# Performance work log

Measured on AMD Instinct MI355X. Metric: run time of the kernel, lower is better.

## Reference

```python
import jax, jax.numpy as jnp
import numpy as np

B, N, DIM = 4, 2048, 64  # batch, seq_len (== gate out dim), model dim (== dim_head)
H, DH = 8, 64            # heads, dim_head


def setup_inputs() -> dict:
    key = jax.random.key(0)
    ks = jax.random.split(key, 12)
    inner = H * DH
    inp = {
        'q': jax.random.normal(ks[0], (B, N, DIM), jnp.float32),
        'k': jax.random.normal(ks[1], (B, N, DIM), jnp.float32),
        'v': jax.random.normal(ks[2], (B, N, DIM), jnp.float32),
        'Wq': jax.random.normal(ks[3], (inner, DIM), jnp.float32) * 0.05,
        'Wk': jax.random.normal(ks[4], (inner, DIM), jnp.float32) * 0.05,
        'Wv': jax.random.normal(ks[5], (inner, DIM), jnp.float32) * 0.05,
        'Wo': jax.random.normal(ks[6], (DIM, inner), jnp.float32) * 0.05,
        'bo': jax.random.normal(ks[7], (DIM,), jnp.float32) * 0.05,
        'Wg': jax.random.normal(ks[8], (N, DIM), jnp.float32) * 0.05,
        's_local': jnp.float32(1.0),
        's_long': jnp.float32(1.0),
        # recurrent compressive-memory state; positive to avoid 0/0 of zero-init buffers
        'mem': jax.random.uniform(ks[9], (H, DH, DH), jnp.float32) + 0.5,
        'mem_norm': jax.random.uniform(ks[10], (H, N, 1), jnp.float32) + 0.5,
    }
    return inp


def _heads(x, W):
    # x: (B,N,DIM) @ W.T (DIM, H*DH) -> (B,H,N,DH)
    y = x @ W.T
    return y.reshape(x.shape[0], x.shape[1], H, DH).transpose(0, 2, 1, 3)


def reference(q, k, v, Wq, Wk, Wv, Wo, bo, Wg, s_local, s_long, mem, mem_norm):
    scale = DH ** -0.5
    qh, kh, vh = _heads(q, Wq), _heads(k, Wk), _heads(v, Wv)  # (B,H,N,DH)

    # local softmax attention, down-gated by (1 - sigmoid(local scalar))
    sim = jnp.einsum('bhnd,bhmd->bhnm', qh, kh) * scale
    local_attn = jax.nn.softmax(sim, axis=-1) * (1.0 - jax.nn.sigmoid(s_local))

    # query compressive memory: elu(q) @ M / (elu(q) * norm)
    eq = jax.nn.elu(qh)
    mem_q = jnp.einsum('bhnd,hde->bhne', eq, mem) / (eq * mem_norm[None])  # (B,H,N,DH)
    gated = jax.nn.sigmoid(s_long) * jnp.einsum('bhnd,md->bhnm', mem_q, Wg)  # (B,H,N,N)

    attn = local_attn + gated
    out = jnp.einsum('bhnm,bhmd->bhnd', attn, vh)
    out = out.transpose(0, 2, 1, 3).reshape(q.shape[0], q.shape[1], H * DH)
    out = out @ Wo.T + bo  # (B,N,DIM)

    # memory update (state side effect in the original forward)
    ek = jax.nn.elu(kh)
    v_term = vh - jnp.einsum('bhnd,hde->bhne', ek, mem) / (ek * mem_norm[None])
    new_mem = mem[None] + jnp.einsum('bhnd,bhne->bhde', ek, v_term)  # (B,H,DH,DH)
    new_norm = ek.sum(-1)  # (B,H,N)
    return out, new_mem, new_norm
```

## Files before the change

### kernel.cpp

```cpp
#include <hip/hip_runtime.h>
#include <math.h>


#define B_   4
#define N_   2048
#define H_   8
#define BH_  32
#define KP   72
#define SCLK 0.18033688f

typedef __bf16 bf16x8 __attribute__((ext_vector_type(8)));
typedef __bf16 bf16x4 __attribute__((ext_vector_type(4)));
typedef short  s16x4  __attribute__((ext_vector_type(4)));
typedef float  f32x4  __attribute__((ext_vector_type(4)));

__device__ __forceinline__ float eluf(float x) {
    return x > 0.0f ? x : expm1f(x);
}

__device__ __forceinline__ float fexp2(float x) {
    return __builtin_amdgcn_exp2f(x);
}

__device__ __forceinline__ f32x4 mfma16(bf16x4 a, bf16x4 b, f32x4 c) {
#if __has_builtin(__builtin_amdgcn_mfma_f32_16x16x16_bf16)
    return __builtin_amdgcn_mfma_f32_16x16x16_bf16(a, b, c, 0, 0, 0);
#else
    s16x4 ai, bi;
    __builtin_memcpy(&ai, &a, 8);
    __builtin_memcpy(&bi, &b, 8);
    return __builtin_amdgcn_mfma_f32_16x16x16bf16_1k(ai, bi, c, 0, 0, 0);
#endif
}

__global__ __launch_bounds__(256) void k_proj(
    const float* __restrict__ q, const float* __restrict__ k, const float* __restrict__ v,
    const float* __restrict__ Wq, const float* __restrict__ Wk, const float* __restrict__ Wv,
    __bf16* __restrict__ qb, float* __restrict__ kh, __bf16* __restrict__ kb,
    __bf16* __restrict__ vb, __bf16* __restrict__ vbT)
{
    const int which = blockIdx.z;
    const int h    = blockIdx.y;
    const int row0 = blockIdx.x * 64;
    const int tid  = threadIdx.x;
    const int b = row0 >> 11, nb = row0 & 2047;

    __shared__ __align__(16) float  AsT[64][68];
    __shared__ __align__(16) float  WsT[64][68];
    __shared__ __align__(16) __bf16 Cs[64 * 72];

    if (which == 2) {
        const int w = tid >> 6, lane = tid & 63;
        const int quad = lane >> 4, m = lane & 15;
        const float* ar = v + (size_t)(row0 + w * 16 + m) * 64;
        bf16x8 a0, a1;
        #pragma unroll
        for (int j = 0; j < 8; ++j) {
            a0[j] = (__bf16)ar[quad * 8 + j];
            a1[j] = (__bf16)ar[32 + quad * 8 + j];
        }
        f32x4 acc[4];
        #pragma unroll
        for (int t = 0; t < 4; ++t) {
            const float* wr = Wv + (size_t)(h * 64 + t * 16 + m) * 64;
            bf16x8 b0, b1;
            #pragma unroll
            for (int j = 0; j < 8; ++j) {
                b0[j] = (__bf16)wr[quad * 8 + j];
                b1[j] = (__bf16)wr[32 + quad * 8 + j];
            }
            f32x4 z = {0.f, 0.f, 0.f, 0.f};
            z = __builtin_amdgcn_mfma_f32_16x16x32_bf16(a0, b0, z, 0, 0, 0);
            acc[t] = __builtin_amdgcn_mfma_f32_16x16x32_bf16(a1, b1, z, 0, 0, 0);
        }
        #pragma unroll
        for (int t = 0; t < 4; ++t)
            #pragma unroll
            for (int r = 0; r < 4; ++r)
                Cs[(w * 16 + quad * 4 + r) * 72 + t * 16 + m] = (__bf16)acc[t][r];
        __syncthreads();
        const int rr = tid >> 2, csg = (tid & 3) * 16;
        bf16x8 r0 = *(const bf16x8*)&Cs[rr * 72 + csg];
        bf16x8 r1 = *(const bf16x8*)&Cs[rr * 72 + csg + 8];
        size_t gb = ((((size_t)b * H_ + h) * N_ + nb + rr) << 6) + csg;
        *(bf16x8*)&vb[gb]     = r0;
        *(bf16x8*)&vb[gb + 8] = r1;
        const int e = tid >> 2, ns = (tid & 3) * 16;
        bf16x8 t0, t1;
        #pragma unroll
        for (int j = 0; j < 8; ++j) {
            t0[j] = Cs[(ns + j) * 72 + e];
            t1[j] = Cs[(ns + 8 + j) * 72 + e];
        }
        size_t base = (((size_t)b * H_ + h) * 64 + e) * (size_t)N_ + nb + ns;
        *(bf16x8*)&vbT[base]     = t0;
        *(bf16x8*)&vbT[base + 8] = t1;
        return;
    }

    const float* __restrict__ src = (which == 0) ? q : k;
    const float* __restrict__ W   = (which == 0) ? Wq : Wk;
    for (int s = 0; s < 16; ++s) {
        int flat = s * 256 + tid;
        int r = flat >> 6, d = flat & 63;
        AsT[d][r] = src[(size_t)(row0 + r) * 64 + d];
        WsT[d][r] = W[(size_t)(h * 64 + r) * 64 + d];
    }
    __syncthreads();

    const int ty = tid >> 4, tx = tid & 15;
    float acc[4][4];
    #pragma unroll
    for (int i = 0; i < 4; ++i)
        #pragma unroll
        for (int j = 0; j < 4; ++j) acc[i][j] = 0.0f;
    for (int kd = 0; kd < 64; ++kd) {
        float4 a4 = *(const float4*)&AsT[kd][ty * 4];
        float4 w4 = *(const float4*)&WsT[kd][tx * 4];
        float a[4] = {a4.x, a4.y, a4.z, a4.w};
        float w[4] = {w4.x, w4.y, w4.z, w4.w};
        #pragma unroll
        for (int i = 0; i < 4; ++i)
            #pragma unroll
            for (int j = 0; j < 4; ++j) acc[i][j] = fmaf(a[i], w[j], acc[i][j]);
    }

    if (which == 0) {
        #pragma unroll
        for (int i = 0; i < 4; ++i) {
            size_t idx = ((((size_t)b * H_ + h) * N_ + nb + ty * 4 + i) << 6) + tx * 4;
            bf16x4 o4 = {(__bf16)acc[i][0], (__bf16)acc[i][1],
                         (__bf16)acc[i][2], (__bf16)acc[i][3]};
            *(bf16x4*)&qb[idx] = o4;
        }
    } else {
        #pragma unroll
        for (int i = 0; i < 4; ++i) {
            size_t idx = ((((size_t)b * H_ + h) * N_ + nb + ty * 4 + i) << 6) + tx * 4;
            *(float4*)&kh[idx] = make_float4(acc[i][0], acc[i][1], acc[i][2], acc[i][3]);
            bf16x4 o4 = {(__bf16)(acc[i][0] * SCLK), (__bf16)(acc[i][1] * SCLK),
                         (__bf16)(acc[i][2] * SCLK), (__bf16)(acc[i][3] * SCLK)};
            *(bf16x4*)&kb[idx] = o4;
        }
    }
}

__global__ __launch_bounds__(256) void k_memacc(
    const float* __restrict__ kh, const __bf16* __restrict__ vb,
    const float* __restrict__ mem, const float* __restrict__ mem_norm,
    float* __restrict__ pmem, float* __restrict__ out_norm)
{
    const int chunk = blockIdx.x;
    const int bh    = blockIdx.y;
    const int h     = bh & 7;
    const int n0    = chunk * 128;

    __shared__ __align__(16) __bf16 memT_hi[64 * KP], memT_lo[64 * KP];
    __shared__ __align__(16) __bf16 ekn_hi[64 * KP],  ekn_lo[64 * KP];
    __shared__ __align__(16) __bf16 ekT_hi[64 * KP],  ekT_lo[64 * KP];
    __shared__ __align__(16) __bf16 vtT_hi[64 * KP],  vtT_lo[64 * KP];

    const int tid  = threadIdx.x;
    const int w    = tid >> 6, lane = tid & 63;
    const int quad = lane >> 4, m = lane & 15;

    for (int s = 0; s < 16; ++s) {
        int flat = s * 256 + tid;
        int d = flat >> 6, e = flat & 63;
        float mv = mem[(size_t)h * 4096 + flat];
        __bf16 hi = (__bf16)mv;
        memT_hi[e * KP + d] = hi;
        memT_lo[e * KP + d] = (__bf16)(mv - (float)hi);
    }

    bf16x8 onesv;
    #pragma unroll
    for (int j = 0; j < 8; ++j) onesv[j] = (m == 0) ? (__bf16)1.0f : (__bf16)0.0f;

    f32x4 accM[4];
    #pragma unroll
    for (int t = 0; t < 4; ++t) { f32x4 z = {0.f, 0.f, 0.f, 0.f}; accM[t] = z; }
    __syncthreads();

    for (int sub = 0; sub < 2; ++sub) {
        const int nb = n0 + sub * 64;
        for (int rr = w; rr < 64; rr += 4) {
            const int n = nb + rr;
            float ekv = eluf(kh[((size_t)bh * N_ + n) * 64 + lane]);
            __bf16 hi = (__bf16)ekv;
            __bf16 lo = (__bf16)(ekv - (float)hi);
            ekn_hi[rr * KP + lane] = hi;
            ekn_lo[rr * KP + lane] = lo;
            ekT_hi[lane * KP + rr] = hi;
            ekT_lo[lane * KP + rr] = lo;
        }
        __syncthreads();

        f32x4 km[4];
        #pragma unroll
        for (int t = 0; t < 4; ++t) { f32x4 z = {0.f, 0.f, 0.f, 0.f}; km[t] = z; }
        f32x4 nsum = {0.f, 0.f, 0.f, 0.f};
        #pragma unroll
        for (int c2 = 0; c2 < 2; ++c2) {
            bf16x8 Ah = *(const bf16x8*)&ekn_hi[(w * 16 + m) * KP + c2 * 32 + quad * 8];
            bf16x8 Al = *(const bf16x8*)&ekn_lo[(w * 16 + m) * KP + c2 * 32 + quad * 8];
            nsum = __builtin_amdgcn_mfma_f32_16x16x32_bf16(Ah, onesv, nsum, 0, 0, 0);
            nsum = __builtin_amdgcn_mfma_f32_16x16x32_bf16(Al, onesv, nsum, 0, 0, 0);
            #pragma unroll
            for (int et = 0; et < 4; ++et) {
                bf16x8 Bh = *(const bf16x8*)&memT_hi[(et * 16 + m) * KP + c2 * 32 + quad * 8];
                bf16x8 Bl = *(const bf16x8*)&memT_lo[(et * 16 + m) * KP + c2 * 32 + quad * 8];
                km[et] = __builtin_amdgcn_mfma_f32_16x16x32_bf16(Al, Bh, km[et], 0, 0, 0);
                km[et] = __builtin_amdgcn_mfma_f32_16x16x32_bf16(Ah, Bl, km[et], 0, 0, 0);
                km[et] = __builtin_amdgcn_mfma_f32_16x16x32_bf16(Ah, Bh, km[et], 0, 0, 0);
            }
        }
        if (m == 0) {
            #pragma unroll
            for (int r = 0; r < 4; ++r)
                out_norm[(size_t)bh * N_ + nb + w * 16 + quad * 4 + r] = nsum[r];
        }
        float nrmv[4];
        #pragma unroll
        for (int r = 0; r < 4; ++r)
            nrmv[r] = mem_norm[(size_t)h * N_ + nb + w * 16 + quad * 4 + r];
        #pragma unroll
        for (int et = 0; et < 4; ++et) {
            #pragma unroll
            for (int r = 0; r < 4; ++r) {
                const int nl = w * 16 + quad * 4 + r;
                const int e  = et * 16 + m;
                float vh  = (float)vb[((size_t)bh * N_ + nb + nl) * 64 + e];
                float ekv = (float)ekn_hi[nl * KP + e] + (float)ekn_lo[nl * KP + e];
                float vt  = vh - km[et][r] * __builtin_amdgcn_rcpf(ekv * nrmv[r]);
                __bf16 hi = (__bf16)vt;
                vtT_hi[e * KP + nl] = hi;
                vtT_lo[e * KP + nl] = (__bf16)(vt - (float)hi);
            }
        }
        __syncthreads();

        #pragma unroll
        for (int c2 = 0; c2 < 2; ++c2) {
            bf16x8 Ah = *(const bf16x8*)&ekT_hi[(w * 16 + m) * KP + c2 * 32 + quad * 8];
            bf16x8 Al = *(const bf16x8*)&ekT_lo[(w * 16 + m) * KP + c2 * 32 + quad * 8];
            #pragma unroll
            for (int et = 0; et < 4; ++et) {
                bf16x8 Bh = *(const bf16x8*)&vtT_hi[(et * 16 + m) * KP + c2 * 32 + quad * 8];
                bf16x8 Bl = *(const bf16x8*)&vtT_lo[(et * 16 + m) * KP + c2 * 32 + quad * 8];
                accM[et] = __builtin_amdgcn_mfma_f32_16x16x32_bf16(Al, Bh, accM[et], 0, 0, 0);
                accM[et] = __builtin_amdgcn_mfma_f32_16x16x32_bf16(Ah, Bl, accM[et], 0, 0, 0);
                accM[et] = __builtin_amdgcn_mfma_f32_16x16x32_bf16(Ah, Bh, accM[et], 0, 0, 0);
            }
        }
        __syncthreads();
    }

    const size_t base = ((size_t)chunk * BH_ + bh) * 4096;
    #pragma unroll
    for (int et = 0; et < 4; ++et)
        #pragma unroll
        for (int r = 0; r < 4; ++r)
            pmem[base + (size_t)(w * 16 + quad * 4 + r) * 64 + et * 16 + m] =
                accM[et][r];
}

__global__ __launch_bounds__(256) void k_gv(
    const float* __restrict__ Wg, const __bf16* __restrict__ vbT,
    float* __restrict__ pGv)
{
    const int chunk = blockIdx.x;
    const int bh    = blockIdx.y;
    const int n0    = chunk * 128;
    __shared__ __align__(16) __bf16 WgT[64 * 136];
    const int tid  = threadIdx.x;
    const int w    = tid >> 6, lane = tid & 63;
    const int quad = lane >> 4, m = tid & 15;

    for (int s = 0; s < 8; ++s) {
        int f4 = s * 256 + tid;
        int n = f4 >> 4, dg = (f4 & 15) * 4;
        float4 wv = *(const float4*)&Wg[(size_t)(n0 + n) * 64 + dg];
        WgT[(dg + 0) * 136 + n] = (__bf16)wv.x;
        WgT[(dg + 1) * 136 + n] = (__bf16)wv.y;
        WgT[(dg + 2) * 136 + n] = (__bf16)wv.z;
        WgT[(dg + 3) * 136 + n] = (__bf16)wv.w;
    }
    __syncthreads();

    f32x4 acc[4];
    #pragma unroll
    for (int t = 0; t < 4; ++t) { f32x4 z = {0.f, 0.f, 0.f, 0.f}; acc[t] = z; }
    #pragma unroll
    for (int c = 0; c < 4; ++c) {
        bf16x8 Af = *(const bf16x8*)&WgT[(w * 16 + m) * 136 + c * 32 + quad * 8];
        #pragma unroll
        for (int et = 0; et < 4; ++et) {
            bf16x8 Bf = *(const bf16x8*)&vbT[((size_t)bh * 64 + et * 16 + m) * N_ +
                                             n0 + c * 32 + quad * 8];
            acc[et] = __builtin_amdgcn_mfma_f32_16x16x32_bf16(Af, Bf, acc[et], 0, 0, 0);
        }
    }
    const size_t base = ((size_t)chunk * BH_ + bh) * 4096;
    #pragma unroll
    for (int et = 0; et < 4; ++et)
        #pragma unroll
        for (int r = 0; r < 4; ++r)
            pGv[base + (size_t)(w * 16 + quad * 4 + r) * 64 + et * 16 + m] =
                acc[et][r];
}

__global__ __launch_bounds__(256) void k_reduce(
    const float* __restrict__ mem, const float* __restrict__ pmem,
    const float* __restrict__ pGv, float* __restrict__ out_mem, float* __restrict__ Gv)
{
    const int idx = blockIdx.x * 256 + threadIdx.x;
    const int bh = idx >> 12, h = bh & 7, de = idx & 4095;
    float sm = mem[(size_t)h * 4096 + de];
    float sg = 0.0f;
    #pragma unroll
    for (int c = 0; c < 16; ++c) {
        sm += pmem[(size_t)c * 131072 + idx];
        sg += pGv[(size_t)c * 131072 + idx];
    }
    out_mem[idx] = sm;
    Gv[idx] = sg;
}

__global__ __launch_bounds__(256, 4) void k_flash(
    const __bf16* __restrict__ qb, const __bf16* __restrict__ kb,
    const __bf16* __restrict__ vbT, const float* __restrict__ mem,
    const float* __restrict__ mem_norm, const float* __restrict__ Gv,
    const float* __restrict__ s_local_p, const float* __restrict__ s_long_p,
    __bf16* __restrict__ o)
{
    const int n0 = blockIdx.x * 128;
    const int bh = blockIdx.y;
    const int h  = bh & 7;
    const __bf16* __restrict__ kbp = kb  + (size_t)bh * N_ * 64;
    const __bf16* __restrict__ vtp = vbT + (size_t)bh * 64 * N_;

    __shared__ __align__(16) __bf16 Kb[64 * KP];
    __shared__ __align__(16) __bf16 VT[64 * KP];
    __shared__ __align__(16) __bf16 Pw[128 * KP];
    __shared__ float lsl[128];
    __shared__ float nrm_l[128];

    const int tid  = threadIdx.x;
    const int w    = tid >> 6, lane = tid & 63;
    const int quad = lane >> 4, m = lane & 15;
    const float gl   = 1.0f - 1.0f / (1.0f + __expf(-s_local_p[0]));
    const float sigg = 1.0f / (1.0f + __expf(-s_long_p[0]));

    if (tid < 128) nrm_l[tid] = mem_norm[(size_t)h * N_ + n0 + tid];

    const size_t q0 = ((size_t)bh * N_ + n0 + w * 32 + m) * 64;
    const size_t q1 = q0 + 16 * 64;
    bf16x8 qa00 = *(const bf16x8*)&qb[q0 + quad * 8];
    bf16x8 qa01 = *(const bf16x8*)&qb[q0 + 32 + quad * 8];
    bf16x8 qa10 = *(const bf16x8*)&qb[q1 + quad * 8];
    bf16x8 qa11 = *(const bf16x8*)&qb[q1 + 32 + quad * 8];

    f32x4 O0[4], O1[4];
    #pragma unroll
    for (int t = 0; t < 4; ++t) {
        f32x4 z = {0.f, 0.f, 0.f, 0.f};
        O0[t] = z; O1[t] = z;
    }
    float lsum0 = 0.f, lsum1 = 0.f;
    const int pr0 = w * 32, pr1 = w * 32 + 16;

    const int srow = tid >> 2, scg = (tid & 3) * 16;
    bf16x8 pk0 = *(const bf16x8*)&kbp[(size_t)srow * 64 + scg];
    bf16x8 pk1 = *(const bf16x8*)&kbp[(size_t)srow * 64 + scg + 8];
    bf16x8 pv0 = *(const bf16x8*)&vtp[(size_t)srow * N_ + scg];
    bf16x8 pv1 = *(const bf16x8*)&vtp[(size_t)srow * N_ + scg + 8];

    for (int c = 0; c < 32; ++c) {
        __syncthreads();
        *(bf16x8*)&Kb[srow * KP + scg]     = pk0;
        *(bf16x8*)&Kb[srow * KP + scg + 8] = pk1;
        *(bf16x8*)&VT[srow * KP + scg]     = pv0;
        *(bf16x8*)&VT[srow * KP + scg + 8] = pv1;
        __syncthreads();
        if (c + 1 < 32) {
            const size_t kn = (size_t)((c + 1) * 64 + srow) * 64 + scg;
            const size_t vn = (size_t)srow * N_ + (c + 1) * 64 + scg;
            pk0 = *(const bf16x8*)&kbp[kn];
            pk1 = *(const bf16x8*)&kbp[kn + 8];
            pv0 = *(const bf16x8*)&vtp[vn];
            pv1 = *(const bf16x8*)&vtp[vn + 8];
        }

        f32x4 s0[4], s1[4];
        #pragma unroll
        for (int t = 0; t < 4; ++t) {
            bf16x8 ka0 = *(const bf16x8*)&Kb[(t * 16 + m) * KP + quad * 8];
            bf16x8 ka1 = *(const bf16x8*)&Kb[(t * 16 + m) * KP + 32 + quad * 8];
            f32x4 z = {0.f, 0.f, 0.f, 0.f};
            z = __builtin_amdgcn_mfma_f32_16x16x32_bf16(ka0, qa00, z, 0, 0, 0);
            s0[t] = __builtin_amdgcn_mfma_f32_16x16x32_bf16(ka1, qa01, z, 0, 0, 0);
            f32x4 z2 = {0.f, 0.f, 0.f, 0.f};
            z2 = __builtin_amdgcn_mfma_f32_16x16x32_bf16(ka0, qa10, z2, 0, 0, 0);
            s1[t] = __builtin_amdgcn_mfma_f32_16x16x32_bf16(ka1, qa11, z2, 0, 0, 0);
        }

        bf16x4 pa0[4], pa1[4];
        #pragma unroll
        for (int t = 0; t < 4; ++t) {
            float p0 = fexp2(s0[t][0]), p1 = fexp2(s0[t][1]);
            float p2 = fexp2(s0[t][2]), p3 = fexp2(s0[t][3]);
            lsum0 += p0 + p1 + p2 + p3;
            bf16x4 pk = {(__bf16)p0, (__bf16)p1, (__bf16)p2, (__bf16)p3};
            pa0[t] = pk;
            float r0 = fexp2(s1[t][0]), r1 = fexp2(s1[t][1]);
            float r2 = fexp2(s1[t][2]), r3 = fexp2(s1[t][3]);
            lsum1 += r0 + r1 + r2 + r3;
            bf16x4 rk = {(__bf16)r0, (__bf16)r1, (__bf16)r2, (__bf16)r3};
            pa1[t] = rk;
        }

        #pragma unroll
        for (int t = 0; t < 4; ++t) {
            #pragma unroll
            for (int et = 0; et < 4; ++et) {
                bf16x4 vb4 = *(const bf16x4*)&VT[(et * 16 + m) * KP + t * 16 + quad * 4];
                O0[et] = mfma16(pa0[t], vb4, O0[et]);
                O1[et] = mfma16(pa1[t], vb4, O1[et]);
            }
        }
    }

    lsum0 += __shfl_xor(lsum0, 16, 64); lsum0 += __shfl_xor(lsum0, 32, 64);
    lsum1 += __shfl_xor(lsum1, 16, 64); lsum1 += __shfl_xor(lsum1, 32, 64);
    if (lane < 16) { lsl[pr0 + lane] = lsum0; lsl[pr1 + lane] = lsum1; }

    __syncthreads();
    for (int s2 = 0; s2 < 16; ++s2) {
        int flat = s2 * 256 + tid;
        int d = flat >> 6, e = flat & 63;
        Kb[e * KP + d] = (__bf16)mem[(size_t)h * 4096 + flat];
        VT[e * KP + d] = (__bf16)Gv[(size_t)bh * 4096 + flat];
    }
    __syncthreads();

    __bf16* op = o + ((size_t)bh * N_ + n0) * 64;
    #pragma unroll
    for (int s = 0; s < 2; ++s) {
        const int prs = w * 32 + s * 16;
        bf16x8 ea0, ea1;
        #pragma unroll
        for (int j = 0; j < 8; ++j) {
            ea0[j] = (__bf16)eluf((float)(s == 0 ? qa00[j] : qa10[j]));
            ea1[j] = (__bf16)eluf((float)(s == 0 ? qa01[j] : qa11[j]));
        }
        f32x4 num[4];
        #pragma unroll
        for (int t = 0; t < 4; ++t) {
            bf16x8 b0 = *(const bf16x8*)&Kb[(t * 16 + m) * KP + quad * 8];
            bf16x8 b1 = *(const bf16x8*)&Kb[(t * 16 + m) * KP + 32 + quad * 8];
            f32x4 z = {0.f, 0.f, 0.f, 0.f};
            z = __builtin_amdgcn_mfma_f32_16x16x32_bf16(ea0, b0, z, 0, 0, 0);
            num[t] = __builtin_amdgcn_mfma_f32_16x16x32_bf16(ea1, b1, z, 0, 0, 0);
        }
        *(bf16x8*)&Pw[(prs + m) * KP + quad * 8]      = ea0;
        *(bf16x8*)&Pw[(prs + m) * KP + 32 + quad * 8] = ea1;
        asm volatile("s_waitcnt lgkmcnt(0)" ::: "memory");
        float mq[4][4];
        #pragma unroll
        for (int t = 0; t < 4; ++t)
            #pragma unroll
            for (int r = 0; r < 4; ++r) {
                float eqv = (float)Pw[(prs + quad * 4 + r) * KP + t * 16 + m];
                mq[t][r] = num[t][r] / (eqv * nrm_l[prs + quad * 4 + r]);
            }
        #pragma unroll
        for (int t = 0; t < 4; ++t)
            #pragma unroll
            for (int r = 0; r < 4; ++r)
                Pw[(prs + quad * 4 + r) * KP + t * 16 + m] = (__bf16)mq[t][r];
        asm volatile("s_waitcnt lgkmcnt(0)" ::: "memory");
        bf16x8 ma0 = *(const bf16x8*)&Pw[(prs + m) * KP + quad * 8];
        bf16x8 ma1 = *(const bf16x8*)&Pw[(prs + m) * KP + 32 + quad * 8];

        #pragma unroll
        for (int t = 0; t < 4; ++t) {
            bf16x8 g0 = *(const bf16x8*)&VT[(t * 16 + m) * KP + quad * 8];
            bf16x8 g1 = *(const bf16x8*)&VT[(t * 16 + m) * KP + 32 + quad * 8];
            f32x4 z = {0.f, 0.f, 0.f, 0.f};
            z = __builtin_amdgcn_mfma_f32_16x16x32_bf16(ma0, g0, z, 0, 0, 0);
            f32x4 o2 = __builtin_amdgcn_mfma_f32_16x16x32_bf16(ma1, g1, z, 0, 0, 0);
            #pragma unroll
            for (int r = 0; r < 4; ++r) {
                const int qr = prs + quad * 4 + r;
                float val = ((s == 0) ? O0[t][r] : O1[t][r]) * (gl / lsl[qr])
                            + sigg * o2[r];
                op[(size_t)qr * 64 + t * 16 + m] = (__bf16)val;
            }
        }
    }
}

__global__ __launch_bounds__(256) void k_outproj(
    const __bf16* __restrict__ o, const float* __restrict__ Wo,
    const float* __restrict__ bo, float* __restrict__ out)
{
    const int row0 = blockIdx.x * 64;
    const int b = row0 >> 11, nb = row0 & 2047;
    __shared__ __align__(16) __bf16 WoS[64 * 40];
    const int tid  = threadIdx.x;
    const int w    = tid >> 6, lane = tid & 63;
    const int quad = lane >> 4, m = lane & 15;

    f32x4 acc[4];
    #pragma unroll
    for (int t = 0; t < 4; ++t) { f32x4 z = {0.f, 0.f, 0.f, 0.f}; acc[t] = z; }

    for (int kbk = 0; kbk < 16; ++kbk) {
        for (int s2 = 0; s2 < 8; ++s2) {
            int flat = s2 * 256 + tid;
            int n = flat >> 5, kk = flat & 31;
            WoS[n * 40 + kk] = (__bf16)Wo[(size_t)n * 512 + kbk * 32 + kk];
        }
        __syncthreads();
        const int hc = kbk >> 1;
        size_t arow = (((size_t)b * H_ + hc) * N_ + nb + w * 16 + m);
        bf16x8 af = *(const bf16x8*)&o[arow * 64 + (kbk & 1) * 32 + quad * 8];
        #pragma unroll
        for (int t = 0; t < 4; ++t) {
            bf16x8 bf_ = *(const bf16x8*)&WoS[(t * 16 + m) * 40 + quad * 8];
            acc[t] = __builtin_amdgcn_mfma_f32_16x16x32_bf16(af, bf_, acc[t], 0, 0, 0);
        }
        __syncthreads();
    }
    #pragma unroll
    for (int t = 0; t < 4; ++t) {
        float bias = bo[t * 16 + m];
        #pragma unroll
        for (int r = 0; r < 4; ++r)
            out[(size_t)(row0 + w * 16 + quad * 4 + r) * 64 + t * 16 + m] =
                acc[t][r] + bias;
    }
}

extern "C" void kernel_launch(void* const* d_in, const int* in_sizes, int n_in,
                              void* d_out, int out_size, void* d_ws, size_t ws_size,
                              hipStream_t stream)
{
    const float* q        = (const float*)d_in[0];
    const float* k        = (const float*)d_in[1];
    const float* v        = (const float*)d_in[2];
    const float* Wq       = (const float*)d_in[3];
    const float* Wk       = (const float*)d_in[4];
    const float* Wv       = (const float*)d_in[5];
    const float* Wo       = (const float*)d_in[6];
    const float* bo       = (const float*)d_in[7];
    const float* Wg       = (const float*)d_in[8];
    const float* s_local  = (const float*)d_in[9];
    const float* s_long   = (const float*)d_in[10];
    const float* mem      = (const float*)d_in[11];
    const float* mem_norm = (const float*)d_in[12];

    float* ws = (float*)d_ws;
    float*  kh  = ws;
    __bf16* qb  = (__bf16*)(ws + 4194304);
    __bf16* kb  = (__bf16*)(ws + 6291456);
    __bf16* vb  = (__bf16*)(ws + 8388608);
    __bf16* vbT = (__bf16*)(ws + 10485760);
    float*  Gv  = ws + 12582912;
    float*  pm  = ws + 12713984;
    float*  pg  = ws + 14811136;
    __bf16* o   = (__bf16*)(ws + 12713984);

    float* out      = (float*)d_out;
    float* out_mem  = out + 524288;
    float* out_norm = out + 655360;

    k_proj   <<<dim3(128, 8, 3), 256, 0, stream>>>(q, k, v, Wq, Wk, Wv,
                                                   qb, kh, kb, vb, vbT);
    k_memacc <<<dim3(16, 32),    256, 0, stream>>>(kh, vb, mem, mem_norm,
                                                   pm, out_norm);
    k_gv     <<<dim3(16, 32),    256, 0, stream>>>(Wg, vbT, pg);
    k_reduce <<<dim3(512),       256, 0, stream>>>(mem, pm, pg, out_mem, Gv);
    k_flash  <<<dim3(16, 32),    256, 0, stream>>>(qb, kb, vbT, mem, mem_norm, Gv,
                                                   s_local, s_long, o);
    k_outproj<<<dim3(128),       256, 0, stream>>>(o, Wo, bo, out);
}
```

Before: 207.7 us.

## Use 512 threads per flash block with one 16-row tile per wave

The flash kernel now launches 512 threads (8 waves) per 128-query block, and each wave handles 16 query rows instead of 32. This halves per-thread accumulators and MFMA work and spreads tile staging across more threads. The idea is to raise wave-level parallelism and latency hiding. The V tile gets a different LDS padding, and the mem/Gv transpose load is rewritten to do vectorized bf16x4 LDS stores. In exchange, K/V tile loads are shared by more waves, each wave does less work per barrier, and register pressure under launch_bounds(512,4) may constrain the compiler.

```diff
diff --git a/kernel.cpp b/kernel.cpp
--- a/kernel.cpp
+++ b/kernel.cpp
@@ -7,6 +7,7 @@
 #define H_   8
 #define BH_  32
 #define KP   72
+#define KPV  68
 #define SCLK 0.18033688f
 
 typedef __bf16 bf16x8 __attribute__((ext_vector_type(8)));
@@ -327,7 +328,7 @@
     Gv[idx] = sg;
 }
 
-__global__ __launch_bounds__(256, 4) void k_flash(
+__global__ __launch_bounds__(512, 4) void k_flash(
     const __bf16* __restrict__ qb, const __bf16* __restrict__ kb,
     const __bf16* __restrict__ vbT, const float* __restrict__ mem,
     const float* __restrict__ mem_norm, const float* __restrict__ Gv,
@@ -341,7 +342,7 @@
     const __bf16* __restrict__ vtp = vbT + (size_t)bh * 64 * N_;
 
     __shared__ __align__(16) __bf16 Kb[64 * KP];
-    __shared__ __align__(16) __bf16 VT[64 * KP];
+    __shared__ __align__(16) __bf16 VT[64 * KPV];
     __shared__ __align__(16) __bf16 Pw[128 * KP];
     __shared__ float lsl[128];
     __shared__ float nrm_l[128];
@@ -354,45 +355,33 @@
 
     if (tid < 128) nrm_l[tid] = mem_norm[(size_t)h * N_ + n0 + tid];
 
-    const size_t q0 = ((size_t)bh * N_ + n0 + w * 32 + m) * 64;
-    const size_t q1 = q0 + 16 * 64;
+    const size_t q0 = ((size_t)bh * N_ + n0 + w * 16 + m) * 64;
     bf16x8 qa00 = *(const bf16x8*)&qb[q0 + quad * 8];
     bf16x8 qa01 = *(const bf16x8*)&qb[q0 + 32 + quad * 8];
-    bf16x8 qa10 = *(const bf16x8*)&qb[q1 + quad * 8];
-    bf16x8 qa11 = *(const bf16x8*)&qb[q1 + 32 + quad * 8];
-
-    f32x4 O0[4], O1[4];
-    #pragma unroll
-    for (int t = 0; t < 4; ++t) {
-        f32x4 z = {0.f, 0.f, 0.f, 0.f};
-        O0[t] = z; O1[t] = z;
-    }
-    float lsum0 = 0.f, lsum1 = 0.f;
-    const int pr0 = w * 32, pr1 = w * 32 + 16;
-
-    const int srow = tid >> 2, scg = (tid & 3) * 16;
+
+    f32x4 O0[4];
+    #pragma unroll
+    for (int t = 0; t < 4; ++t) { f32x4 z = {0.f, 0.f, 0.f, 0.f}; O0[t] = z; }
+    float lsum0 = 0.f;
+    const int prs = w * 16;
+
+    const int srow = tid >> 3, scg = (tid & 7) * 8;
     bf16x8 pk0 = *(const bf16x8*)&kbp[(size_t)srow * 64 + scg];
-    bf16x8 pk1 = *(const bf16x8*)&kbp[(size_t)srow * 64 + scg + 8];
     bf16x8 pv0 = *(const bf16x8*)&vtp[(size_t)srow * N_ + scg];
-    bf16x8 pv1 = *(const bf16x8*)&vtp[(size_t)srow * N_ + scg + 8];
 
     for (int c = 0; c < 32; ++c) {
         __syncthreads();
-        *(bf16x8*)&Kb[srow * KP + scg]     = pk0;
-        *(bf16x8*)&Kb[srow * KP + scg + 8] = pk1;
-        *(bf16x8*)&VT[srow * KP + scg]     = pv0;
-        *(bf16x8*)&VT[srow * KP + scg + 8] = pv1;
+        *(bf16x8*)&Kb[srow * KP + scg]  = pk0;
+        *(bf16x8*)&VT[srow * KPV + scg] = pv0;
         __syncthreads();
         if (c + 1 < 32) {
             const size_t kn = (size_t)((c + 1) * 64 + srow) * 64 + scg;
             const size_t vn = (size_t)srow * N_ + (c + 1) * 64 + scg;
             pk0 = *(const bf16x8*)&kbp[kn];
-            pk1 = *(const bf16x8*)&kbp[kn + 8];
             pv0 = *(const bf16x8*)&vtp[vn];
-            pv1 = *(const bf16x8*)&vtp[vn + 8];
-        }
-
-        f32x4 s0[4], s1[4];
+        }
+
+        f32x4 s0[4];
         #pragma unroll
         for (int t = 0; t < 4; ++t) {
             bf16x8 ka0 = *(const bf16x8*)&Kb[(t * 16 + m) * KP + quad * 8];
@@ -400,12 +389,9 @@
             f32x4 z = {0.f, 0.f, 0.f, 0.f};
             z = __builtin_amdgcn_mfma_f32_16x16x32_bf16(ka0, qa00, z, 0, 0, 0);
             s0[t] = __builtin_amdgcn_mfma_f32_16x16x32_bf16(ka1, qa01, z, 0, 0, 0);
-            f32x4 z2 = {0.f, 0.f, 0.f, 0.f};
-            z2 = __builtin_amdgcn_mfma_f32_16x16x32_bf16(ka0, qa10, z2, 0, 0, 0);
-            s1[t] = __builtin_amdgcn_mfma_f32_16x16x32_bf16(ka1, qa11, z2, 0, 0, 0);
-        }
-
-        bf16x4 pa0[4], pa1[4];
+        }
+
+        bf16x4 pa0[4];
         #pragma unroll
         for (int t = 0; t < 4; ++t) {
             float p0 = fexp2(s0[t][0]), p1 = fexp2(s0[t][1]);
@@ -413,46 +399,49 @@
             lsum0 += p0 + p1 + p2 + p3;
             bf16x4 pk = {(__bf16)p0, (__bf16)p1, (__bf16)p2, (__bf16)p3};
             pa0[t] = pk;
-            float r0 = fexp2(s1[t][0]), r1 = fexp2(s1[t][1]);
-            float r2 = fexp2(s1[t][2]), r3 = fexp2(s1[t][3]);
-            lsum1 += r0 + r1 + r2 + r3;
-            bf16x4 rk = {(__bf16)r0, (__bf16)r1, (__bf16)r2, (__bf16)r3};
-            pa1[t] = rk;
         }
 
         #pragma unroll
         for (int t = 0; t < 4; ++t) {
             #pragma unroll
             for (int et = 0; et < 4; ++et) {
-                bf16x4 vb4 = *(const bf16x4*)&VT[(et * 16 + m) * KP + t * 16 + quad * 4];
+                bf16x4 vb4 = *(const bf16x4*)&VT[(et * 16 + m) * KPV + t * 16 + quad * 4];
                 O0[et] = mfma16(pa0[t], vb4, O0[et]);
-                O1[et] = mfma16(pa1[t], vb4, O1[et]);
-            }
-        }
-    }
-
-    lsum0 += __shfl_xor(lsum0, 16, 64); lsum0 += __shfl_xor(lsum0, 32, 64);
-    lsum1 += __shfl_xor(lsum1, 16, 64); lsum1 += __shfl_xor(lsum1, 32, 64);
-    if (lane < 16) { lsl[pr0 + lane] = lsum0; lsl[pr1 + lane] = lsum1; }
+            }
+        }
+    }
+
+    lsum0 += __shfl_xor(lsum0, 16, 64);
+    lsum0 += __shfl_xor(lsum0, 32, 64);
+    if (lane < 16) lsl[prs + lane] = lsum0;
 
     __syncthreads();
-    for (int s2 = 0; s2 < 16; ++s2) {
-        int flat = s2 * 256 + tid;
-        int d = flat >> 6, e = flat & 63;
-        Kb[e * KP + d] = (__bf16)mem[(size_t)h * 4096 + flat];
-        VT[e * KP + d] = (__bf16)Gv[(size_t)bh * 4096 + flat];
+    {
+        const float* mp = mem + (size_t)h * 4096;
+        const float* gp = Gv + (size_t)bh * 4096;
+        #pragma unroll
+        for (int s2 = 0; s2 < 2; ++s2) {
+            int idx = s2 * 512 + tid;
+            int e = idx & 63, d4 = (idx >> 6) << 2;
+            bf16x4 mv, gv;
+            #pragma unroll
+            for (int j = 0; j < 4; ++j) {
+                mv[j] = (__bf16)mp[(size_t)(d4 + j) * 64 + e];
+                gv[j] = (__bf16)gp[(size_t)(d4 + j) * 64 + e];
+            }
+            *(bf16x4*)&Kb[e * KP + d4]  = mv;
+            *(bf16x4*)&VT[e * KPV + d4] = gv;
+        }
     }
     __syncthreads();
 
     __bf16* op = o + ((size_t)bh * N_ + n0) * 64;
-    #pragma unroll
-    for (int s = 0; s < 2; ++s) {
-        const int prs = w * 32 + s * 16;
+    {
         bf16x8 ea0, ea1;
         #pragma unroll
         for (int j = 0; j < 8; ++j) {
-            ea0[j] = (__bf16)eluf((float)(s == 0 ? qa00[j] : qa10[j]));
-            ea1[j] = (__bf16)eluf((float)(s == 0 ? qa01[j] : qa11[j]));
+            ea0[j] = (__bf16)eluf((float)qa00[j]);
+            ea1[j] = (__bf16)eluf((float)qa01[j]);
         }
         f32x4 num[4];
         #pragma unroll
@@ -485,16 +474,15 @@
 
         #pragma unroll
         for (int t = 0; t < 4; ++t) {
-            bf16x8 g0 = *(const bf16x8*)&VT[(t * 16 + m) * KP + quad * 8];
-            bf16x8 g1 = *(const bf16x8*)&VT[(t * 16 + m) * KP + 32 + quad * 8];
+            bf16x8 g0 = *(const bf16x8*)&VT[(t * 16 + m) * KPV + quad * 8];
+            bf16x8 g1 = *(const bf16x8*)&VT[(t * 16 + m) * KPV + 32 + quad * 8];
             f32x4 z = {0.f, 0.f, 0.f, 0.f};
             z = __builtin_amdgcn_mfma_f32_16x16x32_bf16(ma0, g0, z, 0, 0, 0);
             f32x4 o2 = __builtin_amdgcn_mfma_f32_16x16x32_bf16(ma1, g1, z, 0, 0, 0);
             #pragma unroll
             for (int r = 0; r < 4; ++r) {
                 const int qr = prs + quad * 4 + r;
-                float val = ((s == 0) ? O0[t][r] : O1[t][r]) * (gl / lsl[qr])
-                            + sigg * o2[r];
+                float val = O0[t][r] * (gl / lsl[qr]) + sigg * o2[r];
                 op[(size_t)qr * 64 + t * 16 + m] = (__bf16)val;
             }
         }
@@ -582,7 +570,7 @@
                                                    pm, out_norm);
     k_gv     <<<dim3(16, 32),    256, 0, stream>>>(Wg, vbT, pg);
     k_reduce <<<dim3(512),       256, 0, stream>>>(mem, pm, pg, out_mem, Gv);
-    k_flash  <<<dim3(16, 32),    256, 0, stream>>>(qb, kb, vbT, mem, mem_norm, Gv,
+    k_flash  <<<dim3(16, 32),    512, 0, stream>>>(qb, kb, vbT, mem, mem_norm, Gv,
                                                    s_local, s_long, o);
     k_outproj<<<dim3(128),       256, 0, stream>>>(o, Wo, bo, out);
 }
```

After: 201.2 us. -3.2%, faster.

## Double-buffer K/V tiles in flash kernel and enlarge blocks to 512 threads

Applied to the files above, without the earlier changes.

The flash-attention kernel now processes 256 query rows per 512-thread block. K and V^T tiles sit in ping-pong LDS buffers, so each key chunk needs one barrier instead of two, and global prefetch runs two chunks ahead. The V tile uses a narrower padding stride, and the memory/Gv transpose into LDS is rewritten to issue 4-element vector stores. LDS is carved from one shared byte array with aliased regions for the epilogue. The larger LDS footprint and bigger blocks reduce block count and may limit occupancy.

```diff
diff --git a/kernel.cpp b/kernel.cpp
--- a/kernel.cpp
+++ b/kernel.cpp
@@ -7,6 +7,7 @@
 #define H_   8
 #define BH_  32
 #define KP   72
+#define KPV  68
 #define SCLK 0.18033688f
 
 typedef __bf16 bf16x8 __attribute__((ext_vector_type(8)));
@@ -327,24 +328,29 @@
     Gv[idx] = sg;
 }
 
-__global__ __launch_bounds__(256, 4) void k_flash(
+__global__ __launch_bounds__(512, 2) void k_flash(
     const __bf16* __restrict__ qb, const __bf16* __restrict__ kb,
     const __bf16* __restrict__ vbT, const float* __restrict__ mem,
     const float* __restrict__ mem_norm, const float* __restrict__ Gv,
     const float* __restrict__ s_local_p, const float* __restrict__ s_long_p,
     __bf16* __restrict__ o)
 {
-    const int n0 = blockIdx.x * 128;
+    const int n0 = blockIdx.x * 256;
     const int bh = blockIdx.y;
     const int h  = bh & 7;
     const __bf16* __restrict__ kbp = kb  + (size_t)bh * N_ * 64;
     const __bf16* __restrict__ vtp = vbT + (size_t)bh * 64 * N_;
 
-    __shared__ __align__(16) __bf16 Kb[64 * KP];
-    __shared__ __align__(16) __bf16 VT[64 * KP];
-    __shared__ __align__(16) __bf16 Pw[128 * KP];
-    __shared__ float lsl[128];
-    __shared__ float nrm_l[128];
+    __shared__ __align__(16) char smem[56832];
+    __bf16* const KbA = (__bf16*)(smem);
+    __bf16* const KbB = (__bf16*)(smem + 9216);
+    __bf16* const VTA = (__bf16*)(smem + 18432);
+    __bf16* const VTB = (__bf16*)(smem + 27136);
+    __bf16* const MT  = (__bf16*)(smem);
+    __bf16* const GT  = (__bf16*)(smem + 9216);
+    __bf16* const Pw  = (__bf16*)(smem + 17920);
+    float*  const lsl   = (float*)(smem + 54784);
+    float*  const nrm_l = (float*)(smem + 55808);
 
     const int tid  = threadIdx.x;
     const int w    = tid >> 6, lane = tid & 63;
@@ -352,7 +358,7 @@
     const float gl   = 1.0f - 1.0f / (1.0f + __expf(-s_local_p[0]));
     const float sigg = 1.0f / (1.0f + __expf(-s_long_p[0]));
 
-    if (tid < 128) nrm_l[tid] = mem_norm[(size_t)h * N_ + n0 + tid];
+    if (tid < 256) nrm_l[tid] = mem_norm[(size_t)h * N_ + n0 + tid];
 
     const size_t q0 = ((size_t)bh * N_ + n0 + w * 32 + m) * 64;
     const size_t q1 = q0 + 16 * 64;
@@ -370,33 +376,40 @@
     float lsum0 = 0.f, lsum1 = 0.f;
     const int pr0 = w * 32, pr1 = w * 32 + 16;
 
-    const int srow = tid >> 2, scg = (tid & 3) * 16;
+    const int srow = tid >> 3, scg = (tid & 7) * 8;
     bf16x8 pk0 = *(const bf16x8*)&kbp[(size_t)srow * 64 + scg];
-    bf16x8 pk1 = *(const bf16x8*)&kbp[(size_t)srow * 64 + scg + 8];
     bf16x8 pv0 = *(const bf16x8*)&vtp[(size_t)srow * N_ + scg];
-    bf16x8 pv1 = *(const bf16x8*)&vtp[(size_t)srow * N_ + scg + 8];
+    *(bf16x8*)&KbA[srow * KP + scg]  = pk0;
+    *(bf16x8*)&VTA[srow * KPV + scg] = pv0;
+    {
+        const size_t kn = (size_t)(64 + srow) * 64 + scg;
+        const size_t vn = (size_t)srow * N_ + 64 + scg;
+        pk0 = *(const bf16x8*)&kbp[kn];
+        pv0 = *(const bf16x8*)&vtp[vn];
+    }
 
     for (int c = 0; c < 32; ++c) {
         __syncthreads();
-        *(bf16x8*)&Kb[srow * KP + scg]     = pk0;
-        *(bf16x8*)&Kb[srow * KP + scg + 8] = pk1;
-        *(bf16x8*)&VT[srow * KP + scg]     = pv0;
-        *(bf16x8*)&VT[srow * KP + scg + 8] = pv1;
-        __syncthreads();
         if (c + 1 < 32) {
-            const size_t kn = (size_t)((c + 1) * 64 + srow) * 64 + scg;
-            const size_t vn = (size_t)srow * N_ + (c + 1) * 64 + scg;
+            __bf16* Kn = (c & 1) ? KbA : KbB;
+            __bf16* Vn = (c & 1) ? VTA : VTB;
+            *(bf16x8*)&Kn[srow * KP + scg]  = pk0;
+            *(bf16x8*)&Vn[srow * KPV + scg] = pv0;
+        }
+        if (c + 2 < 32) {
+            const size_t kn = (size_t)((c + 2) * 64 + srow) * 64 + scg;
+            const size_t vn = (size_t)srow * N_ + (c + 2) * 64 + scg;
             pk0 = *(const bf16x8*)&kbp[kn];
-            pk1 = *(const bf16x8*)&kbp[kn + 8];
             pv0 = *(const bf16x8*)&vtp[vn];
-            pv1 = *(const bf16x8*)&vtp[vn + 8];
-        }
+        }
+        const __bf16* Kc = (c & 1) ? KbB : KbA;
+        const __bf16* Vc = (c & 1) ? VTB : VTA;
 
         f32x4 s0[4], s1[4];
         #pragma unroll
         for (int t = 0; t < 4; ++t) {
-            bf16x8 ka0 = *(const bf16x8*)&Kb[(t * 16 + m) * KP + quad * 8];
-            bf16x8 ka1 = *(const bf16x8*)&Kb[(t * 16 + m) * KP + 32 + quad * 8];
+            bf16x8 ka0 = *(const bf16x8*)&Kc[(t * 16 + m) * KP + quad * 8];
+            bf16x8 ka1 = *(const bf16x8*)&Kc[(t * 16 + m) * KP + 32 + quad * 8];
             f32x4 z = {0.f, 0.f, 0.f, 0.f};
             z = __builtin_amdgcn_mfma_f32_16x16x32_bf16(ka0, qa00, z, 0, 0, 0);
             s0[t] = __builtin_amdgcn_mfma_f32_16x16x32_bf16(ka1, qa01, z, 0, 0, 0);
@@ -424,7 +437,7 @@
         for (int t = 0; t < 4; ++t) {
             #pragma unroll
             for (int et = 0; et < 4; ++et) {
-                bf16x4 vb4 = *(const bf16x4*)&VT[(et * 16 + m) * KP + t * 16 + quad * 4];
+                bf16x4 vb4 = *(const bf16x4*)&Vc[(et * 16 + m) * KPV + t * 16 + quad * 4];
                 O0[et] = mfma16(pa0[t], vb4, O0[et]);
                 O1[et] = mfma16(pa1[t], vb4, O1[et]);
             }
@@ -436,11 +449,22 @@
     if (lane < 16) { lsl[pr0 + lane] = lsum0; lsl[pr1 + lane] = lsum1; }
 
     __syncthreads();
-    for (int s2 = 0; s2 < 16; ++s2) {
-        int flat = s2 * 256 + tid;
-        int d = flat >> 6, e = flat & 63;
-        Kb[e * KP + d] = (__bf16)mem[(size_t)h * 4096 + flat];
-        VT[e * KP + d] = (__bf16)Gv[(size_t)bh * 4096 + flat];
+    {
+        const float* mp = mem + (size_t)h * 4096;
+        const float* gp = Gv + (size_t)bh * 4096;
+        #pragma unroll
+        for (int s2 = 0; s2 < 2; ++s2) {
+            int idx = s2 * 512 + tid;
+            int e = idx & 63, d4 = (idx >> 6) << 2;
+            bf16x4 mv, gv;
+            #pragma unroll
+            for (int j = 0; j < 4; ++j) {
+                mv[j] = (__bf16)mp[(size_t)(d4 + j) * 64 + e];
+                gv[j] = (__bf16)gp[(size_t)(d4 + j) * 64 + e];
+            }
+            *(bf16x4*)&MT[e * KP + d4] = mv;
+            *(bf16x4*)&GT[e * KPV + d4] = gv;
+        }
     }
     __syncthreads();
 
@@ -457,8 +481,8 @@
         f32x4 num[4];
         #pragma unroll
         for (int t = 0; t < 4; ++t) {
-            bf16x8 b0 = *(const bf16x8*)&Kb[(t * 16 + m) * KP + quad * 8];
-            bf16x8 b1 = *(const bf16x8*)&Kb[(t * 16 + m) * KP + 32 + quad * 8];
+            bf16x8 b0 = *(const bf16x8*)&MT[(t * 16 + m) * KP + quad * 8];
+            bf16x8 b1 = *(const bf16x8*)&MT[(t * 16 + m) * KP + 32 + quad * 8];
             f32x4 z = {0.f, 0.f, 0.f, 0.f};
             z = __builtin_amdgcn_mfma_f32_16x16x32_bf16(ea0, b0, z, 0, 0, 0);
             num[t] = __builtin_amdgcn_mfma_f32_16x16x32_bf16(ea1, b1, z, 0, 0, 0);
@@ -485,8 +509,8 @@
 
         #pragma unroll
         for (int t = 0; t < 4; ++t) {
-            bf16x8 g0 = *(const bf16x8*)&VT[(t * 16 + m) * KP + quad * 8];
-            bf16x8 g1 = *(const bf16x8*)&VT[(t * 16 + m) * KP + 32 + quad * 8];
+            bf16x8 g0 = *(const bf16x8*)&GT[(t * 16 + m) * KPV + quad * 8];
+            bf16x8 g1 = *(const bf16x8*)&GT[(t * 16 + m) * KPV + 32 + quad * 8];
             f32x4 z = {0.f, 0.f, 0.f, 0.f};
             z = __builtin_amdgcn_mfma_f32_16x16x32_bf16(ma0, g0, z, 0, 0, 0);
             f32x4 o2 = __builtin_amdgcn_mfma_f32_16x16x32_bf16(ma1, g1, z, 0, 0, 0);
@@ -582,7 +606,7 @@
                                                    pm, out_norm);
     k_gv     <<<dim3(16, 32),    256, 0, stream>>>(Wg, vbT, pg);
     k_reduce <<<dim3(512),       256, 0, stream>>>(mem, pm, pg, out_mem, Gv);
-    k_flash  <<<dim3(16, 32),    256, 0, stream>>>(qb, kb, vbT, mem, mem_norm, Gv,
+    k_flash  <<<dim3(8, 32),     512, 0, stream>>>(qb, kb, vbT, mem, mem_norm, Gv,
                                                    s_local, s_long, o);
     k_outproj<<<dim3(128),       256, 0, stream>>>(o, Wo, bo, out);
 }
```

Result: faster. 198.8 us (-4.3%).
